# Kernel optimization log

Hardware: AMD Instinct MI355X
Metric: run time of the kernel (lower is better)

Reference implementation:

```python
import jax, jax.numpy as jnp
import numpy as np

V, D, H, L, S_MAX, FF = 32000, 1024, 16, 6, 1024, 4096
HD = D // H
EPS = 1e-5

def _ln(x, g, b):
    mu = jnp.mean(x, axis=-1, keepdims=True)
    var = jnp.mean((x - mu) ** 2, axis=-1, keepdims=True)
    return (x - mu) * jax.lax.rsqrt(var + EPS) * g + b

def setup_inputs() -> dict:
    key = jax.random.key(0)
    ks = jax.random.split(key, 12)
    std = 0.02
    d = {}
    d['x'] = jax.random.randint(ks[0], (2, 1024), 0, V)
    d['tok_emb'] = std * jax.random.normal(ks[1], (V, D), jnp.float32)
    d['pos_emb'] = std * jax.random.normal(ks[2], (S_MAX, D), jnp.float32)
    d['ln1_g'] = jnp.ones((L, D)); d['ln1_b'] = jnp.zeros((L, D))
    d['qkv_w'] = std * jax.random.normal(ks[3], (L, 3 * D, D), jnp.float32)
    d['qkv_b'] = jnp.zeros((L, 3 * D))
    d['proj_w'] = std * jax.random.normal(ks[4], (L, D, D), jnp.float32)
    d['proj_b'] = jnp.zeros((L, D))
    d['ln2_g'] = jnp.ones((L, D)); d['ln2_b'] = jnp.zeros((L, D))
    d['fc1_w'] = std * jax.random.normal(ks[5], (L, FF, D), jnp.float32)
    d['fc1_b'] = jnp.zeros((L, FF))
    d['fc2_w'] = std * jax.random.normal(ks[6], (L, D, FF), jnp.float32)
    d['fc2_b'] = jnp.zeros((L, D))
    d['lnf_g'] = jnp.ones((D,)); d['lnf_b'] = jnp.zeros((D,))
    d['head_w'] = std * jax.random.normal(ks[7], (V, D), jnp.float32)
    return d

def _gpt(x, tok_emb, pos_emb, ln1_g, ln1_b, qkv_w, qkv_b, proj_w, proj_b,
         ln2_g, ln2_b, fc1_w, fc1_b, fc2_w, fc2_b, lnf_g, lnf_b, head_w):
    B, S = x.shape
    h = tok_emb[x] + pos_emb[:S][None]  # (B,S,D)
    scale = HD ** -0.5
    causal = jnp.tril(jnp.ones((S, S), bool))
    neg_inf = jnp.finfo(h.dtype).min

    def block(h, p):
        l1g, l1b, qw, qb, pw, pb, l2g, l2b, f1w, f1b, f2w, f2b = p
        xn = _ln(h, l1g, l1b)
        qkv = xn @ qw.T + qb  # (B,S,3D)
        qkv = qkv.reshape(B, S, 3, H, HD).transpose(2, 0, 3, 1, 4)  # (3,B,H,S,HD)
        q, k, v = qkv[0], qkv[1], qkv[2]
        scores = jnp.einsum('bhqd,bhkd->bhqk', q, k) * scale
        scores = jnp.where(causal, scores, neg_inf)
        attn = jax.nn.softmax(scores, axis=-1)
        o = jnp.einsum('bhqk,bhkd->bhqd', attn, v)
        o = o.transpose(0, 2, 1, 3).reshape(B, S, D)
        h = h + (o @ pw.T + pb)
        xn = _ln(h, l2g, l2b)
        ff = jax.nn.gelu(xn @ f1w.T + f1b, approximate=False) @ f2w.T + f2b
        return h + ff, None

    params = (ln1_g, ln1_b, qkv_w, qkv_b, proj_w, proj_b,
              ln2_g, ln2_b, fc1_w, fc1_b, fc2_w, fc2_b)
    h, _ = jax.lax.scan(block, h, params)
    h = _ln(h, lnf_g, lnf_b)
    return h @ head_w.T  # (B,S,V)

def reference(x, tok_emb, pos_emb, ln1_g, ln1_b, qkv_w, qkv_b, proj_w, proj_b,
              ln2_g, ln2_b, fc1_w, fc1_b, fc2_w, fc2_b, lnf_g, lnf_b, head_w):
    return _gpt(x, tok_emb, pos_emb, ln1_g, ln1_b, qkv_w, qkv_b, proj_w, proj_b,
                ln2_g, ln2_b, fc1_w, fc1_b, fc2_w, fc2_b, lnf_g, lnf_b, head_w)
```

## Files before the change

kernel.cpp:

```cpp
#include <hip/hip_runtime.h>

typedef unsigned short u16;
typedef unsigned int   u32;
typedef __bf16 bf16x8 __attribute__((ext_vector_type(8)));
typedef float  f32x4  __attribute__((ext_vector_type(4)));

#define DEV __device__ __forceinline__

DEV u16 f2bf(float f) {
    u32 u = __builtin_bit_cast(u32, f);
    u32 r = u + 0x7FFFu + ((u >> 16) & 1u);
    return (u16)(r >> 16);
}

DEV void gload16(const void* g, void* l) {
    __builtin_amdgcn_global_load_lds((const __attribute__((address_space(1))) void*)g,
                                     (__attribute__((address_space(3))) void*)l, 16, 0, 0);
}

DEV int xcd_swz(int bid, int nwg) {
    int q = nwg >> 3, r = nwg & 7;
    int xcd = bid & 7, idx = bid >> 3;
    return (xcd < r ? xcd * (q + 1) : r * (q + 1) + (xcd - r) * q) + idx;
}

DEV int swz(int p) {
    int m = (((p >> 7) & 1) << 6) | (((p >> 9) & 1) << 5) | (((p >> 8) & 1) << 4);
    return p ^ m;
}

__global__ void cvt_k(const float* __restrict__ src, u16* __restrict__ dst, int n4) {
    int i = blockIdx.x * blockDim.x + threadIdx.x;
    int stride = gridDim.x * blockDim.x;
    for (; i < n4; i += stride) {
        float4 v = ((const float4*)src)[i];
        ushort4 u;
        u.x = f2bf(v.x); u.y = f2bf(v.y); u.z = f2bf(v.z); u.w = f2bf(v.w);
        ((ushort4*)dst)[i] = u;
    }
}

__global__ void cvt4_k(const float* __restrict__ s0, const float* __restrict__ s1,
                       const float* __restrict__ s2, const float* __restrict__ s3,
                       u16* __restrict__ dst, int n0, int n1, int n2, int n3) {
    int i = blockIdx.x * blockDim.x + threadIdx.x;
    int stride = gridDim.x * blockDim.x;
    int t0 = n0, t1 = t0 + n1, t2 = t1 + n2, t3 = t2 + n3;
    for (; i < t3; i += stride) {
        const float* s; int j;
        if (i < t0)      { s = s0; j = i; }
        else if (i < t1) { s = s1; j = i - t0; }
        else if (i < t2) { s = s2; j = i - t1; }
        else             { s = s3; j = i - t2; }
        float4 v = ((const float4*)s)[j];
        ushort4 u;
        u.x = f2bf(v.x); u.y = f2bf(v.y); u.z = f2bf(v.z); u.w = f2bf(v.w);
        ((ushort4*)dst)[i] = u;
    }
}

__global__ void embed_k(const int* __restrict__ x, const float* __restrict__ te,
                        const float* __restrict__ pe, float* __restrict__ h) {
    int row = blockIdx.x;
    int t = threadIdx.x;
    int tok = x[row];
    int s = row & 1023;
    float4 a = ((const float4*)(te + (size_t)tok * 1024))[t];
    float4 p = ((const float4*)(pe + (size_t)s * 1024))[t];
    a.x += p.x; a.y += p.y; a.z += p.z; a.w += p.w;
    ((float4*)(h + (size_t)row * 1024))[t] = a;
}

__global__ void ln_k(const float* __restrict__ in, const float* __restrict__ g,
                     const float* __restrict__ b, u16* __restrict__ out) {
    int row = blockIdx.x;
    int t = threadIdx.x;
    float4 v = ((const float4*)(in + (size_t)row * 1024))[t];
    float s = v.x + v.y + v.z + v.w;
    float s2 = v.x * v.x + v.y * v.y + v.z * v.z + v.w * v.w;
    #pragma unroll
    for (int msk = 1; msk < 64; msk <<= 1) {
        s  += __shfl_xor(s, msk);
        s2 += __shfl_xor(s2, msk);
    }
    __shared__ float ps[4], ps2[4];
    if ((t & 63) == 0) { ps[t >> 6] = s; ps2[t >> 6] = s2; }
    __syncthreads();
    s = ps[0] + ps[1] + ps[2] + ps[3];
    s2 = ps2[0] + ps2[1] + ps2[2] + ps2[3];
    float mu = s * (1.0f / 1024.0f);
    float var = s2 * (1.0f / 1024.0f) - mu * mu;
    float rstd = rsqrtf(var + 1e-5f);
    float4 gg = ((const float4*)g)[t];
    float4 bb = ((const float4*)b)[t];
    ushort4 o;
    o.x = f2bf((v.x - mu) * rstd * gg.x + bb.x);
    o.y = f2bf((v.y - mu) * rstd * gg.y + bb.y);
    o.z = f2bf((v.z - mu) * rstd * gg.z + bb.z);
    o.w = f2bf((v.w - mu) * rstd * gg.w + bb.w);
    ((ushort4*)out)[(size_t)row * 256 + t] = o;
}

__global__ void fuse2_k(const float* __restrict__ p0, const float* __restrict__ p1,
                        const float* __restrict__ bias, float* __restrict__ h) {
    int row = blockIdx.x;
    int t = threadIdx.x;
    size_t idx = (size_t)row * 256 + t;
    float4 a = ((const float4*)p0)[idx];
    float4 b = ((const float4*)p1)[idx];
    float4 c = ((const float4*)bias)[t];
    float4 v = ((const float4*)h)[idx];
    v.x += a.x + b.x + c.x;
    v.y += a.y + b.y + c.y;
    v.z += a.z + b.z + c.z;
    v.w += a.w + b.w + c.w;
    ((float4*)h)[idx] = v;
}

template<int PH>
DEV void phase_mma(const bf16x8 (&af)[2][2], const bf16x8 (&bfr)[4][2], f32x4 (&acc)[8][4]) {
    __builtin_amdgcn_s_barrier();
    asm volatile("s_waitcnt lgkmcnt(0)" ::: "memory");
    __builtin_amdgcn_sched_barrier(0);
    __builtin_amdgcn_s_setprio(1);
    #pragma unroll
    for (int ms = 0; ms < 2; ++ms)
        #pragma unroll
        for (int nj = 0; nj < 4; ++nj)
            #pragma unroll
            for (int kk = 0; kk < 2; ++kk)
                acc[PH * 2 + ms][nj] = __builtin_amdgcn_mfma_f32_16x16x32_bf16(
                    af[ms][kk], bfr[nj][kk], acc[PH * 2 + ms][nj], 0, 0, 0);
    __builtin_amdgcn_s_setprio(0);
}

template<int PH>
DEV void read_afrags(const char* Ab, int arow, int fr, int fq, bf16x8 (&af)[2][2]) {
    #pragma unroll
    for (int ms = 0; ms < 2; ++ms)
        #pragma unroll
        for (int kk = 0; kk < 2; ++kk) {
            int lin = (arow + (PH * 2 + ms) * 16 + fr) * 128 + kk * 64 + fq * 16;
            af[ms][kk] = *(const bf16x8*)(Ab + swz(lin));
        }
}

template<int BIAS, int OUTBF>
__global__ __launch_bounds__(512, 2)
void gemm8p(const u16* __restrict__ A, const u16* __restrict__ Bw,
            const float* __restrict__ bias,
            float* __restrict__ outf, u16* __restrict__ outb,
            int M, int N, int K) {
    __shared__ char lds[131072];
    char* ldsA = lds;
    char* ldsB = lds + 65536;
    const int t = threadIdx.x;
    const int w = t >> 6, l = t & 63;
    const int fr = l & 15, fq = l >> 4;
    const int wm = w >> 2, wn = w & 3;

    int bid = blockIdx.y * gridDim.x + blockIdx.x;
    int swzb = xcd_swz(bid, gridDim.x * gridDim.y);
    const int m0 = (swzb % gridDim.x) * 256;
    const int n0 = (swzb / gridDim.x) * 256;
    const int nt = K >> 6;
    const int arow = wm * 128;

    const u16* Asrc = A + (size_t)m0 * K;
    const u16* Bsrc = Bw + (size_t)n0 * K;

    size_t o00, o01, o10, o11;
    {
        int p;
        p = 0 * 16384 + 0 * 8192 + t * 16; o00 = (size_t)(p >> 7) * K + ((swz(p) & 127) >> 1);
        p = 0 * 16384 + 1 * 8192 + t * 16; o01 = (size_t)(p >> 7) * K + ((swz(p) & 127) >> 1);
        p = 1 * 16384 + 0 * 8192 + t * 16; o10 = (size_t)(p >> 7) * K + ((swz(p) & 127) >> 1);
        p = 1 * 16384 + 1 * 8192 + t * 16; o11 = (size_t)(p >> 7) * K + ((swz(p) & 127) >> 1);
    }
    const int wb = w * 1024;

    gload16(Asrc + o00, ldsA + wb);
    gload16(Asrc + o01, ldsA + 8192 + wb);
    gload16(Asrc + o10, ldsA + 16384 + wb);
    gload16(Asrc + o11, ldsA + 16384 + 8192 + wb);
    gload16(Bsrc + o00, ldsB + wb);
    gload16(Bsrc + o01, ldsB + 8192 + wb);
    gload16(Bsrc + o10, ldsB + 16384 + wb);
    gload16(Bsrc + o11, ldsB + 16384 + 8192 + wb);
    gload16(Bsrc + o00 + 64, ldsB + 32768 + wb);
    gload16(Bsrc + o01 + 64, ldsB + 32768 + 8192 + wb);
    gload16(Bsrc + o10 + 64, ldsB + 32768 + 16384 + wb);
    gload16(Bsrc + o11 + 64, ldsB + 32768 + 16384 + 8192 + wb);
    asm volatile("s_waitcnt vmcnt(4)" ::: "memory");
    __builtin_amdgcn_s_barrier();
    __builtin_amdgcn_sched_barrier(0);

    f32x4 acc[8][4] = {};

    for (int T = 0; T < nt; ++T) {
        const char* Ab = ldsA + (T & 1) * 32768;
        const char* Bb = ldsB + (T & 1) * 32768;
        char* Anx = ldsA + ((T + 1) & 1) * 32768;
        char* Bnx = ldsB + (T & 1) * 32768;
        const bool stA = (T + 1 < nt), stB = (T + 2 < nt);
        const size_t kA = (size_t)(T + 1) * 64, kB = (size_t)(T + 2) * 64;

        bf16x8 bfr[4][2], af[2][2];

        #pragma unroll
        for (int nj = 0; nj < 4; ++nj)
            #pragma unroll
            for (int kk = 0; kk < 2; ++kk) {
                int lin = (wn * 64 + nj * 16 + fr) * 128 + kk * 64 + fq * 16;
                bfr[nj][kk] = *(const bf16x8*)(Bb + swz(lin));
            }
        read_afrags<0>(Ab, arow, fr, fq, af);
        if (stA) {
            gload16(Asrc + o00 + kA, Anx + wb);
            gload16(Asrc + o01 + kA, Anx + 8192 + wb);
        }
        phase_mma<0>(af, bfr, acc);
        __builtin_amdgcn_s_barrier();

        read_afrags<1>(Ab, arow, fr, fq, af);
        if (stA) {
            gload16(Asrc + o10 + kA, Anx + 16384 + wb);
            gload16(Asrc + o11 + kA, Anx + 16384 + 8192 + wb);
        }
        phase_mma<1>(af, bfr, acc);
        __builtin_amdgcn_s_barrier();

        read_afrags<2>(Ab, arow, fr, fq, af);
        if (stB) {
            gload16(Bsrc + o00 + kB, Bnx + wb);
            gload16(Bsrc + o01 + kB, Bnx + 8192 + wb);
        }
        phase_mma<2>(af, bfr, acc);
        __builtin_amdgcn_s_barrier();

        read_afrags<3>(Ab, arow, fr, fq, af);
        if (stB) {
            gload16(Bsrc + o10 + kB, Bnx + 16384 + wb);
            gload16(Bsrc + o11 + kB, Bnx + 16384 + 8192 + wb);
        }
        phase_mma<3>(af, bfr, acc);
        if (stB)      asm volatile("s_waitcnt vmcnt(4)" ::: "memory");
        else if (stA) asm volatile("s_waitcnt vmcnt(0)" ::: "memory");
        __builtin_amdgcn_s_barrier();
        __builtin_amdgcn_sched_barrier(0);
    }

    #pragma unroll
    for (int mi = 0; mi < 8; ++mi) {
        #pragma unroll
        for (int nj = 0; nj < 4; ++nj) {
            #pragma unroll
            for (int r = 0; r < 4; ++r) {
                int row = m0 + wm * 128 + mi * 16 + fq * 4 + r;
                int col = n0 + wn * 64 + nj * 16 + fr;
                float v = acc[mi][nj][r];
                if (BIAS) v += bias[col];
                if (OUTBF) outb[(size_t)row * N + col] = f2bf(v);
                else       outf[(size_t)row * N + col] = v;
            }
        }
    }
}

template<int BIAS, int GELU_, int OUTBF, int SPLITK>
__global__ __launch_bounds__(512, 2)
void gemm4p(const u16* __restrict__ A, const u16* __restrict__ Bw,
            const float* __restrict__ bias,
            float* __restrict__ outf, u16* __restrict__ outb,
            int M, int N, int K) {
    __shared__ char lds[65536];
    char* ldsA = lds;
    char* ldsB = lds + 32768;
    const int t = threadIdx.x;
    const int w = t >> 6, l = t & 63;
    const int fr = l & 15, fq = l >> 4;
    const int wm = w >> 2, wn = w & 3;

    int bid = blockIdx.y * gridDim.x + blockIdx.x;
    int swzb = xcd_swz(bid, gridDim.x * gridDim.y);
    const int m0 = (swzb % gridDim.x) * 128;
    const int n0 = (swzb / gridDim.x) * 128;

    int kbase = 0, Keff = K;
    if (SPLITK) { Keff = K >> 1; kbase = blockIdx.z * Keff; }
    const int nt = Keff >> 6;

    const u16* Asrc = A + (size_t)m0 * K + kbase;
    const u16* Bsrc = Bw + (size_t)n0 * K + kbase;

    size_t o0, o1;
    {
        int p = t * 16;        o0 = (size_t)(p >> 7) * K + ((swz(p) & 127) >> 1);
        p = 8192 + t * 16;     o1 = (size_t)(p >> 7) * K + ((swz(p) & 127) >> 1);
    }
    const int wb = w * 1024;

    gload16(Asrc + o0, ldsA + wb);
    gload16(Asrc + o1, ldsA + 8192 + wb);
    gload16(Bsrc + o0, ldsB + wb);
    gload16(Bsrc + o1, ldsB + 8192 + wb);
    gload16(Bsrc + o0 + 64, ldsB + 16384 + wb);
    gload16(Bsrc + o1 + 64, ldsB + 16384 + 8192 + wb);
    asm volatile("s_waitcnt vmcnt(2)" ::: "memory");
    __builtin_amdgcn_s_barrier();
    __builtin_amdgcn_sched_barrier(0);

    f32x4 acc[4][2] = {};

    for (int T = 0; T < nt; ++T) {
        const char* Ab = ldsA + (T & 1) * 16384;
        const char* Bb = ldsB + (T & 1) * 16384;
        char* Anx = ldsA + ((T + 1) & 1) * 16384;
        char* Bnx = ldsB + (T & 1) * 16384;
        const bool stA = (T + 1 < nt), stB = (T + 2 < nt);
        const size_t kA = (size_t)(T + 1) * 64, kB = (size_t)(T + 2) * 64;

        bf16x8 bfr[2][2], af[2][2];

        #pragma unroll
        for (int nj = 0; nj < 2; ++nj)
            #pragma unroll
            for (int kk = 0; kk < 2; ++kk) {
                int lin = (wn * 32 + nj * 16 + fr) * 128 + kk * 64 + fq * 16;
                bfr[nj][kk] = *(const bf16x8*)(Bb + swz(lin));
            }
        #pragma unroll
        for (int ms = 0; ms < 2; ++ms)
            #pragma unroll
            for (int kk = 0; kk < 2; ++kk) {
                int lin = (wm * 64 + ms * 16 + fr) * 128 + kk * 64 + fq * 16;
                af[ms][kk] = *(const bf16x8*)(Ab + swz(lin));
            }
        if (stA) {
            gload16(Asrc + o0 + kA, Anx + wb);
            gload16(Asrc + o1 + kA, Anx + 8192 + wb);
        }
        __builtin_amdgcn_s_barrier();
        asm volatile("s_waitcnt lgkmcnt(0)" ::: "memory");
        __builtin_amdgcn_sched_barrier(0);
        __builtin_amdgcn_s_setprio(1);
        #pragma unroll
        for (int ms = 0; ms < 2; ++ms)
            #pragma unroll
            for (int nj = 0; nj < 2; ++nj)
                #pragma unroll
                for (int kk = 0; kk < 2; ++kk)
                    acc[ms][nj] = __builtin_amdgcn_mfma_f32_16x16x32_bf16(
                        af[ms][kk], bfr[nj][kk], acc[ms][nj], 0, 0, 0);
        __builtin_amdgcn_s_setprio(0);
        __builtin_amdgcn_s_barrier();

        #pragma unroll
        for (int ms = 0; ms < 2; ++ms)
            #pragma unroll
            for (int kk = 0; kk < 2; ++kk) {
                int lin = (wm * 64 + (2 + ms) * 16 + fr) * 128 + kk * 64 + fq * 16;
                af[ms][kk] = *(const bf16x8*)(Ab + swz(lin));
            }
        if (stB) {
            gload16(Bsrc + o0 + kB, Bnx + wb);
            gload16(Bsrc + o1 + kB, Bnx + 8192 + wb);
        }
        __builtin_amdgcn_s_barrier();
        asm volatile("s_waitcnt lgkmcnt(0)" ::: "memory");
        __builtin_amdgcn_sched_barrier(0);
        __builtin_amdgcn_s_setprio(1);
        #pragma unroll
        for (int ms = 0; ms < 2; ++ms)
            #pragma unroll
            for (int nj = 0; nj < 2; ++nj)
                #pragma unroll
                for (int kk = 0; kk < 2; ++kk)
                    acc[2 + ms][nj] = __builtin_amdgcn_mfma_f32_16x16x32_bf16(
                        af[ms][kk], bfr[nj][kk], acc[2 + ms][nj], 0, 0, 0);
        __builtin_amdgcn_s_setprio(0);
        if (stB)      asm volatile("s_waitcnt vmcnt(2)" ::: "memory");
        else if (stA) asm volatile("s_waitcnt vmcnt(0)" ::: "memory");
        __builtin_amdgcn_s_barrier();
        __builtin_amdgcn_sched_barrier(0);
    }

    float* op = outf;
    if (SPLITK) op = outf + (size_t)blockIdx.z * M * N;

    #pragma unroll
    for (int mi = 0; mi < 4; ++mi) {
        #pragma unroll
        for (int nj = 0; nj < 2; ++nj) {
            #pragma unroll
            for (int r = 0; r < 4; ++r) {
                int row = m0 + wm * 64 + mi * 16 + fq * 4 + r;
                int col = n0 + wn * 32 + nj * 16 + fr;
                float v = acc[mi][nj][r];
                if (BIAS) v += bias[col];
                if (GELU_) v = 0.5f * v * (1.0f + erff(v * 0.70710678118f));
                if (OUTBF) outb[(size_t)row * N + col] = f2bf(v);
                else       op[(size_t)row * N + col] = v;
            }
        }
    }
}

template<int BM, int BN, int BIAS, int GELU_, int RES, int OUTBF, int SPLITK>
__global__ void gemm_db(const u16* __restrict__ A, const u16* __restrict__ Bw,
                        const float* __restrict__ bias, const float* __restrict__ res,
                        float* __restrict__ outf, u16* __restrict__ outb,
                        int M, int N, int K) {
    constexpr int MR = BM / 32;
    constexpr int NR = BN / 32;
    constexpr int AL = BM / 64;
    constexpr int BL = BN / 64;
    __shared__ u16 lA[2][BM * 32];
    __shared__ u16 lB[2][BN * 32];
    const int t = threadIdx.x;
    const int w = t >> 6, l = t & 63;

    int bid = blockIdx.y * gridDim.x + blockIdx.x;
    int swzb = xcd_swz(bid, gridDim.x * gridDim.y);
    const int m0 = (swzb % gridDim.x) * BM;
    const int n0 = (swzb / gridDim.x) * BN;

    int kbase = 0, Keff = K;
    if (SPLITK) { Keff = K >> 1; kbase = blockIdx.z * Keff; }
    const int nt = Keff >> 5;

    const int wr = (w >> 1) * (BM / 2), wc = (w & 1) * (BN / 2);
    const int fr = l & 15, fq = l >> 4;
    const int g0 = w * 64 + l;

    const int srow = g0 >> 2, scol = (g0 & 3) * 8;

    f32x4 acc[MR][NR] = {};

    #pragma unroll
    for (int i = 0; i < AL; ++i)
        gload16(A + (size_t)(m0 + srow + i * 64) * K + kbase + scol, lA[0] + (srow + i * 64) * 32 + scol);
    #pragma unroll
    for (int i = 0; i < BL; ++i)
        gload16(Bw + (size_t)(n0 + srow + i * 64) * K + kbase + scol, lB[0] + (srow + i * 64) * 32 + scol);
    __syncthreads();

    for (int T = 0; T < nt; ++T) {
        const int cur = T & 1, nxt = cur ^ 1;
        if (T + 1 < nt) {
            const int kk = kbase + (T + 1) * 32;
            #pragma unroll
            for (int i = 0; i < AL; ++i)
                gload16(A + (size_t)(m0 + srow + i * 64) * K + kk + scol, lA[nxt] + (srow + i * 64) * 32 + scol);
            #pragma unroll
            for (int i = 0; i < BL; ++i)
                gload16(Bw + (size_t)(n0 + srow + i * 64) * K + kk + scol, lB[nxt] + (srow + i * 64) * 32 + scol);
        }
        bf16x8 af[MR], bfv[NR];
        #pragma unroll
        for (int mi = 0; mi < MR; ++mi)
            af[mi] = *(const bf16x8*)(lA[cur] + (wr + mi * 16 + fr) * 32 + fq * 8);
        #pragma unroll
        for (int ni = 0; ni < NR; ++ni)
            bfv[ni] = *(const bf16x8*)(lB[cur] + (wc + ni * 16 + fr) * 32 + fq * 8);
        #pragma unroll
        for (int mi = 0; mi < MR; ++mi)
            #pragma unroll
            for (int ni = 0; ni < NR; ++ni)
                acc[mi][ni] = __builtin_amdgcn_mfma_f32_16x16x32_bf16(af[mi], bfv[ni], acc[mi][ni], 0, 0, 0);
        __syncthreads();
    }

    float* op = outf;
    if (SPLITK) op = outf + (size_t)blockIdx.z * M * N;

    #pragma unroll
    for (int mi = 0; mi < MR; ++mi) {
        #pragma unroll
        for (int ni = 0; ni < NR; ++ni) {
            #pragma unroll
            for (int r = 0; r < 4; ++r) {
                int row = m0 + wr + mi * 16 + fq * 4 + r;
                int col = n0 + wc + ni * 16 + fr;
                float v = acc[mi][ni][r];
                if (BIAS) v += bias[col];
                if (GELU_) v = 0.5f * v * (1.0f + erff(v * 0.70710678118f));
                if (RES) v += res[(size_t)row * N + col];
                if (OUTBF) outb[(size_t)row * N + col] = f2bf(v);
                else       op[(size_t)row * N + col] = v;
            }
        }
    }
}

__global__ __launch_bounds__(512, 2)
void attn_k(const u16* __restrict__ qkv, u16* __restrict__ o) {
    __shared__ u16 lK[64 * 64];
    __shared__ u16 lV[64 * 64];
    __shared__ u16 lP[8 * 16 * 64];
    const int t = threadIdx.x;
    const int w = t >> 6, l = t & 63;
    const int fr = l & 15, fq = l >> 4;

    int swzb = xcd_swz(blockIdx.x, gridDim.x);
    const int qb = 7 - (swzb & 7);
    const int hh = (swzb >> 3) & 15;
    const int b  = swzb >> 7;
    const int q0 = qb * 128;
    const int qw = q0 + w * 16;

    const u16* srcK;
    {
        int p = t * 16;
        int L = swz(p);
        srcK = qkv + ((size_t)(b * 1024) + (L >> 7)) * 3072 + 1024 + hh * 64 + ((L & 127) >> 1);
    }

    bf16x8 qf[2];
    {
        size_t base = ((size_t)(b * 1024) + qw + fr) * 3072 + hh * 64;
        qf[0] = *(const bf16x8*)(qkv + base + fq * 8);
        qf[1] = *(const bf16x8*)(qkv + base + 32 + fq * 8);
    }

    float m_run[4], l_run[4];
    f32x4 acc_o[4] = {};
    #pragma unroll
    for (int r = 0; r < 4; ++r) { m_run[r] = -__builtin_inff(); l_run[r] = 0.0f; }

    for (int kv0 = 0; kv0 < q0 + 128; kv0 += 64) {
        gload16(srcK + (size_t)kv0 * 3072, (char*)lK + w * 1024);
        {
            int kv = t >> 3, d0 = (t & 7) * 8;
            const u32* gv = (const u32*)(qkv + ((size_t)(b * 1024) + kv0 + kv) * 3072 + 2048 + hh * 64 + d0);
            u32 v0 = gv[0], v1 = gv[1], v2 = gv[2], v3 = gv[3];
            u16 e[8] = { (u16)v0, (u16)(v0 >> 16), (u16)v1, (u16)(v1 >> 16),
                         (u16)v2, (u16)(v2 >> 16), (u16)v3, (u16)(v3 >> 16) };
            #pragma unroll
            for (int j = 0; j < 8; ++j) {
                int pv = ((d0 + j) * 64 + kv) * 2;
                *(u16*)((char*)lV + swz(pv)) = e[j];
            }
        }
        __syncthreads();

        const bool active = (kv0 <= qw + 15);
        if (active) {
            f32x4 accs[4] = {};
            #pragma unroll
            for (int nt = 0; nt < 4; ++nt) {
                #pragma unroll
                for (int ks = 0; ks < 2; ++ks) {
                    int pk = ((nt * 16 + fr) * 64 + ks * 32 + fq * 8) * 2;
                    bf16x8 kf = *(const bf16x8*)((const char*)lK + swz(pk));
                    accs[nt] = __builtin_amdgcn_mfma_f32_16x16x32_bf16(qf[ks], kf, accs[nt], 0, 0, 0);
                }
            }

            float p[4][4], mx[4], rs[4];
            #pragma unroll
            for (int r = 0; r < 4; ++r) {
                int qg = qw + fq * 4 + r;
                float m = -__builtin_inff();
                #pragma unroll
                for (int nt = 0; nt < 4; ++nt) {
                    int kvg = kv0 + nt * 16 + fr;
                    float s = (kvg <= qg) ? accs[nt][r] * 0.125f : -__builtin_inff();
                    p[nt][r] = s;
                    m = fmaxf(m, s);
                }
                mx[r] = m;
            }
            #pragma unroll
            for (int msk = 1; msk < 16; msk <<= 1) {
                #pragma unroll
                for (int r = 0; r < 4; ++r) mx[r] = fmaxf(mx[r], __shfl_xor(mx[r], msk));
            }
            float mnew[4], alpha[4];
            #pragma unroll
            for (int r = 0; r < 4; ++r) {
                mnew[r] = fmaxf(m_run[r], mx[r]);
                alpha[r] = __expf(m_run[r] - mnew[r]);
                float s = 0.0f;
                #pragma unroll
                for (int nt = 0; nt < 4; ++nt) {
                    float pv = __expf(p[nt][r] - mnew[r]);
                    p[nt][r] = pv;
                    s += pv;
                }
                rs[r] = s;
            }
            #pragma unroll
            for (int msk = 1; msk < 16; msk <<= 1) {
                #pragma unroll
                for (int r = 0; r < 4; ++r) rs[r] += __shfl_xor(rs[r], msk);
            }
            #pragma unroll
            for (int r = 0; r < 4; ++r) {
                l_run[r] = l_run[r] * alpha[r] + rs[r];
                m_run[r] = mnew[r];
            }
            #pragma unroll
            for (int nt = 0; nt < 4; ++nt)
                #pragma unroll
                for (int r = 0; r < 4; ++r) acc_o[nt][r] *= alpha[r];

            #pragma unroll
            for (int nt = 0; nt < 4; ++nt)
                #pragma unroll
                for (int r = 0; r < 4; ++r) {
                    int pp = (w * 1024 + (fq * 4 + r) * 64 + nt * 16 + fr) * 2;
                    *(u16*)((char*)lP + swz(pp)) = f2bf(p[nt][r]);
                }

            bf16x8 pa[2];
            #pragma unroll
            for (int ks = 0; ks < 2; ++ks) {
                int ppr = (w * 1024 + fr * 64 + ks * 32 + fq * 8) * 2;
                pa[ks] = *(const bf16x8*)((const char*)lP + swz(ppr));
            }
            #pragma unroll
            for (int nt = 0; nt < 4; ++nt) {
                #pragma unroll
                for (int ks = 0; ks < 2; ++ks) {
                    int pvr = ((nt * 16 + fr) * 64 + ks * 32 + fq * 8) * 2;
                    bf16x8 vf = *(const bf16x8*)((const char*)lV + swz(pvr));
                    acc_o[nt] = __builtin_amdgcn_mfma_f32_16x16x32_bf16(pa[ks], vf, acc_o[nt], 0, 0, 0);
                }
            }
        }
        __syncthreads();
    }

    #pragma unroll
    for (int nt = 0; nt < 4; ++nt) {
        #pragma unroll
        for (int r = 0; r < 4; ++r) {
            int qg = qw + fq * 4 + r;
            int d = nt * 16 + fr;
            float ov = acc_o[nt][r] / l_run[r];
            o[((size_t)(b * 1024) + qg) * 1024 + hh * 64 + d] = f2bf(ov);
        }
    }
}

extern "C" void kernel_launch(void* const* d_in, const int* in_sizes, int n_in,
                              void* d_out, int out_size, void* d_ws, size_t ws_size,
                              hipStream_t stream) {
    const int*   x       = (const int*)  d_in[0];
    const float* tok_emb = (const float*)d_in[1];
    const float* pos_emb = (const float*)d_in[2];
    const float* ln1_g   = (const float*)d_in[3];
    const float* ln1_b   = (const float*)d_in[4];
    const float* qkv_w   = (const float*)d_in[5];
    const float* qkv_b   = (const float*)d_in[6];
    const float* proj_w  = (const float*)d_in[7];
    const float* proj_b  = (const float*)d_in[8];
    const float* ln2_g   = (const float*)d_in[9];
    const float* ln2_b   = (const float*)d_in[10];
    const float* fc1_w   = (const float*)d_in[11];
    const float* fc1_b   = (const float*)d_in[12];
    const float* fc2_w   = (const float*)d_in[13];
    const float* fc2_b   = (const float*)d_in[14];
    const float* lnf_g   = (const float*)d_in[15];
    const float* lnf_b   = (const float*)d_in[16];
    const float* head_w  = (const float*)d_in[17];
    float* out = (float*)d_out;

    char* ws = (char*)d_ws;
    float* h   = (float*)(ws + 0);
    u16*   xn  = (u16*)(ws + 8388608);
    u16*   qkv = (u16*)(ws + 12582912);
    u16*   ob  = (u16*)(ws + 25165824);
    u16*   ff  = (u16*)(ws + 29360128);
    u16*   wq  = (u16*)(ws + 46137344);
    float* pbuf = (float*)(ws + 12582912);

    u16* wqkv = wq;
    u16* wproj = wqkv + 3072 * 1024;
    u16* wfc1  = wproj + 1024 * 1024;
    u16* wfc2  = wfc1 + 4096 * 1024;

    const int M = 2048;

    embed_k<<<dim3(2048), 256, 0, stream>>>(x, tok_emb, pos_emb, h);

    for (int lyr = 0; lyr < 6; ++lyr) {
        cvt4_k<<<dim3(2048), 256, 0, stream>>>(
            qkv_w + (size_t)lyr * 3072 * 1024, proj_w + (size_t)lyr * 1024 * 1024,
            fc1_w + (size_t)lyr * 4096 * 1024, fc2_w + (size_t)lyr * 1024 * 4096,
            wq, 3072 * 256, 1024 * 256, 4096 * 256, 4096 * 256);
        ln_k<<<dim3(2048), 256, 0, stream>>>(h, ln1_g + lyr * 1024, ln1_b + lyr * 1024, xn);
        gemm4p<1, 0, 1, 0><<<dim3(16, 24), 512, 0, stream>>>(
            xn, wqkv, qkv_b + lyr * 3072, nullptr, qkv, M, 3072, 1024);
        attn_k<<<dim3(256), 512, 0, stream>>>(qkv, ob);
        gemm_db<64, 64, 1, 0, 1, 0, 0><<<dim3(32, 16), 256, 0, stream>>>(
            ob, wproj, proj_b + lyr * 1024, h, h, nullptr, M, 1024, 1024);
        ln_k<<<dim3(2048), 256, 0, stream>>>(h, ln2_g + lyr * 1024, ln2_b + lyr * 1024, xn);
        gemm4p<1, 1, 1, 0><<<dim3(16, 32), 512, 0, stream>>>(
            xn, wfc1, fc1_b + lyr * 4096, nullptr, ff, M, 4096, 1024);
        gemm4p<0, 0, 0, 1><<<dim3(16, 8, 2), 512, 0, stream>>>(
            ff, wfc2, nullptr, pbuf, nullptr, M, 1024, 4096);
        fuse2_k<<<dim3(2048), 256, 0, stream>>>(
            pbuf, pbuf + (size_t)M * 1024, fc2_b + lyr * 1024, h);
    }

    ln_k<<<dim3(2048), 256, 0, stream>>>(h, lnf_g, lnf_b, xn);
    cvt_k<<<dim3(2048), 256, 0, stream>>>(head_w, wq, 32000 * 1024 / 4);
    gemm8p<0, 0><<<dim3(8, 125), 512, 0, stream>>>(
        xn, wq, nullptr, out, nullptr, M, 32000, 1024);
}
```

Measured before the change: 1.256 ms.

## Fuse LayerNorm into embedding and residual-reduce kernels; use gemm4p for head

LayerNorm is computed inside the embedding kernel and inside the split-K residual reduction kernel, which now also produces the next layer's normalized input (or the final LN). This removes the standalone LN launches and the extra passes over the fp32 hidden state. The vocabulary projection switches from the large-tile gemm8p kernel to the smaller-tile gemm4p kernel, and gemm8p is deleted. Smaller tiles raise global traffic for the head GEMM but may improve occupancy and load balance.

```diff
diff --git a/kernel.cpp b/kernel.cpp
--- a/kernel.cpp
+++ b/kernel.cpp
@@ -59,23 +59,8 @@
     }
 }
 
-__global__ void embed_k(const int* __restrict__ x, const float* __restrict__ te,
-                        const float* __restrict__ pe, float* __restrict__ h) {
-    int row = blockIdx.x;
-    int t = threadIdx.x;
-    int tok = x[row];
-    int s = row & 1023;
-    float4 a = ((const float4*)(te + (size_t)tok * 1024))[t];
-    float4 p = ((const float4*)(pe + (size_t)s * 1024))[t];
-    a.x += p.x; a.y += p.y; a.z += p.z; a.w += p.w;
-    ((float4*)(h + (size_t)row * 1024))[t] = a;
-}
-
-__global__ void ln_k(const float* __restrict__ in, const float* __restrict__ g,
-                     const float* __restrict__ b, u16* __restrict__ out) {
-    int row = blockIdx.x;
-    int t = threadIdx.x;
-    float4 v = ((const float4*)(in + (size_t)row * 1024))[t];
+DEV void ln_store(float4 v, const float* __restrict__ g, const float* __restrict__ b,
+                  u16* __restrict__ out, int row, int t) {
     float s = v.x + v.y + v.z + v.w;
     float s2 = v.x * v.x + v.y * v.y + v.z * v.z + v.w * v.w;
     #pragma unroll
@@ -101,170 +86,46 @@
     ((ushort4*)out)[(size_t)row * 256 + t] = o;
 }
 
-__global__ void fuse2_k(const float* __restrict__ p0, const float* __restrict__ p1,
-                        const float* __restrict__ bias, float* __restrict__ h) {
+__global__ void ln_k(const float* __restrict__ in, const float* __restrict__ g,
+                     const float* __restrict__ b, u16* __restrict__ out) {
+    int row = blockIdx.x;
+    int t = threadIdx.x;
+    float4 v = ((const float4*)(in + (size_t)row * 1024))[t];
+    ln_store(v, g, b, out, row, t);
+}
+
+__global__ void embed_ln_k(const int* __restrict__ x, const float* __restrict__ te,
+                           const float* __restrict__ pe, float* __restrict__ h,
+                           const float* __restrict__ g, const float* __restrict__ b,
+                           u16* __restrict__ xn) {
+    int row = blockIdx.x;
+    int t = threadIdx.x;
+    int tok = x[row];
+    int s = row & 1023;
+    float4 a = ((const float4*)(te + (size_t)tok * 1024))[t];
+    float4 p = ((const float4*)(pe + (size_t)s * 1024))[t];
+    a.x += p.x; a.y += p.y; a.z += p.z; a.w += p.w;
+    ((float4*)(h + (size_t)row * 1024))[t] = a;
+    ln_store(a, g, b, xn, row, t);
+}
+
+__global__ void fuse2ln_k(const float* __restrict__ p0, const float* __restrict__ p1,
+                          const float* __restrict__ bias, float* __restrict__ h,
+                          const float* __restrict__ g, const float* __restrict__ b,
+                          u16* __restrict__ xn) {
     int row = blockIdx.x;
     int t = threadIdx.x;
     size_t idx = (size_t)row * 256 + t;
     float4 a = ((const float4*)p0)[idx];
-    float4 b = ((const float4*)p1)[idx];
+    float4 bb = ((const float4*)p1)[idx];
     float4 c = ((const float4*)bias)[t];
     float4 v = ((const float4*)h)[idx];
-    v.x += a.x + b.x + c.x;
-    v.y += a.y + b.y + c.y;
-    v.z += a.z + b.z + c.z;
-    v.w += a.w + b.w + c.w;
+    v.x += a.x + bb.x + c.x;
+    v.y += a.y + bb.y + c.y;
+    v.z += a.z + bb.z + c.z;
+    v.w += a.w + bb.w + c.w;
     ((float4*)h)[idx] = v;
-}
-
-template<int PH>
-DEV void phase_mma(const bf16x8 (&af)[2][2], const bf16x8 (&bfr)[4][2], f32x4 (&acc)[8][4]) {
-    __builtin_amdgcn_s_barrier();
-    asm volatile("s_waitcnt lgkmcnt(0)" ::: "memory");
-    __builtin_amdgcn_sched_barrier(0);
-    __builtin_amdgcn_s_setprio(1);
-    #pragma unroll
-    for (int ms = 0; ms < 2; ++ms)
-        #pragma unroll
-        for (int nj = 0; nj < 4; ++nj)
-            #pragma unroll
-            for (int kk = 0; kk < 2; ++kk)
-                acc[PH * 2 + ms][nj] = __builtin_amdgcn_mfma_f32_16x16x32_bf16(
-                    af[ms][kk], bfr[nj][kk], acc[PH * 2 + ms][nj], 0, 0, 0);
-    __builtin_amdgcn_s_setprio(0);
-}
-
-template<int PH>
-DEV void read_afrags(const char* Ab, int arow, int fr, int fq, bf16x8 (&af)[2][2]) {
-    #pragma unroll
-    for (int ms = 0; ms < 2; ++ms)
-        #pragma unroll
-        for (int kk = 0; kk < 2; ++kk) {
-            int lin = (arow + (PH * 2 + ms) * 16 + fr) * 128 + kk * 64 + fq * 16;
-            af[ms][kk] = *(const bf16x8*)(Ab + swz(lin));
-        }
-}
-
-template<int BIAS, int OUTBF>
-__global__ __launch_bounds__(512, 2)
-void gemm8p(const u16* __restrict__ A, const u16* __restrict__ Bw,
-            const float* __restrict__ bias,
-            float* __restrict__ outf, u16* __restrict__ outb,
-            int M, int N, int K) {
-    __shared__ char lds[131072];
-    char* ldsA = lds;
-    char* ldsB = lds + 65536;
-    const int t = threadIdx.x;
-    const int w = t >> 6, l = t & 63;
-    const int fr = l & 15, fq = l >> 4;
-    const int wm = w >> 2, wn = w & 3;
-
-    int bid = blockIdx.y * gridDim.x + blockIdx.x;
-    int swzb = xcd_swz(bid, gridDim.x * gridDim.y);
-    const int m0 = (swzb % gridDim.x) * 256;
-    const int n0 = (swzb / gridDim.x) * 256;
-    const int nt = K >> 6;
-    const int arow = wm * 128;
-
-    const u16* Asrc = A + (size_t)m0 * K;
-    const u16* Bsrc = Bw + (size_t)n0 * K;
-
-    size_t o00, o01, o10, o11;
-    {
-        int p;
-        p = 0 * 16384 + 0 * 8192 + t * 16; o00 = (size_t)(p >> 7) * K + ((swz(p) & 127) >> 1);
-        p = 0 * 16384 + 1 * 8192 + t * 16; o01 = (size_t)(p >> 7) * K + ((swz(p) & 127) >> 1);
-        p = 1 * 16384 + 0 * 8192 + t * 16; o10 = (size_t)(p >> 7) * K + ((swz(p) & 127) >> 1);
-        p = 1 * 16384 + 1 * 8192 + t * 16; o11 = (size_t)(p >> 7) * K + ((swz(p) & 127) >> 1);
-    }
-    const int wb = w * 1024;
-
-    gload16(Asrc + o00, ldsA + wb);
-    gload16(Asrc + o01, ldsA + 8192 + wb);
-    gload16(Asrc + o10, ldsA + 16384 + wb);
-    gload16(Asrc + o11, ldsA + 16384 + 8192 + wb);
-    gload16(Bsrc + o00, ldsB + wb);
-    gload16(Bsrc + o01, ldsB + 8192 + wb);
-    gload16(Bsrc + o10, ldsB + 16384 + wb);
-    gload16(Bsrc + o11, ldsB + 16384 + 8192 + wb);
-    gload16(Bsrc + o00 + 64, ldsB + 32768 + wb);
-    gload16(Bsrc + o01 + 64, ldsB + 32768 + 8192 + wb);
-    gload16(Bsrc + o10 + 64, ldsB + 32768 + 16384 + wb);
-    gload16(Bsrc + o11 + 64, ldsB + 32768 + 16384 + 8192 + wb);
-    asm volatile("s_waitcnt vmcnt(4)" ::: "memory");
-    __builtin_amdgcn_s_barrier();
-    __builtin_amdgcn_sched_barrier(0);
-
-    f32x4 acc[8][4] = {};
-
-    for (int T = 0; T < nt; ++T) {
-        const char* Ab = ldsA + (T & 1) * 32768;
-        const char* Bb = ldsB + (T & 1) * 32768;
-        char* Anx = ldsA + ((T + 1) & 1) * 32768;
-        char* Bnx = ldsB + (T & 1) * 32768;
-        const bool stA = (T + 1 < nt), stB = (T + 2 < nt);
-        const size_t kA = (size_t)(T + 1) * 64, kB = (size_t)(T + 2) * 64;
-
-        bf16x8 bfr[4][2], af[2][2];
-
-        #pragma unroll
-        for (int nj = 0; nj < 4; ++nj)
-            #pragma unroll
-            for (int kk = 0; kk < 2; ++kk) {
-                int lin = (wn * 64 + nj * 16 + fr) * 128 + kk * 64 + fq * 16;
-                bfr[nj][kk] = *(const bf16x8*)(Bb + swz(lin));
-            }
-        read_afrags<0>(Ab, arow, fr, fq, af);
-        if (stA) {
-            gload16(Asrc + o00 + kA, Anx + wb);
-            gload16(Asrc + o01 + kA, Anx + 8192 + wb);
-        }
-        phase_mma<0>(af, bfr, acc);
-        __builtin_amdgcn_s_barrier();
-
-        read_afrags<1>(Ab, arow, fr, fq, af);
-        if (stA) {
-            gload16(Asrc + o10 + kA, Anx + 16384 + wb);
-            gload16(Asrc + o11 + kA, Anx + 16384 + 8192 + wb);
-        }
-        phase_mma<1>(af, bfr, acc);
-        __builtin_amdgcn_s_barrier();
-
-        read_afrags<2>(Ab, arow, fr, fq, af);
-        if (stB) {
-            gload16(Bsrc + o00 + kB, Bnx + wb);
-            gload16(Bsrc + o01 + kB, Bnx + 8192 + wb);
-        }
-        phase_mma<2>(af, bfr, acc);
-        __builtin_amdgcn_s_barrier();
-
-        read_afrags<3>(Ab, arow, fr, fq, af);
-        if (stB) {
-            gload16(Bsrc + o10 + kB, Bnx + 16384 + wb);
-            gload16(Bsrc + o11 + kB, Bnx + 16384 + 8192 + wb);
-        }
-        phase_mma<3>(af, bfr, acc);
-        if (stB)      asm volatile("s_waitcnt vmcnt(4)" ::: "memory");
-        else if (stA) asm volatile("s_waitcnt vmcnt(0)" ::: "memory");
-        __builtin_amdgcn_s_barrier();
-        __builtin_amdgcn_sched_barrier(0);
-    }
-
-    #pragma unroll
-    for (int mi = 0; mi < 8; ++mi) {
-        #pragma unroll
-        for (int nj = 0; nj < 4; ++nj) {
-            #pragma unroll
-            for (int r = 0; r < 4; ++r) {
-                int row = m0 + wm * 128 + mi * 16 + fq * 4 + r;
-                int col = n0 + wn * 64 + nj * 16 + fr;
-                float v = acc[mi][nj][r];
-                if (BIAS) v += bias[col];
-                if (OUTBF) outb[(size_t)row * N + col] = f2bf(v);
-                else       outf[(size_t)row * N + col] = v;
-            }
-        }
-    }
+    ln_store(v, g, b, xn, row, t);
 }
 
 template<int BIAS, int GELU_, int OUTBF, int SPLITK>
@@ -683,14 +544,13 @@
 
     const int M = 2048;
 
-    embed_k<<<dim3(2048), 256, 0, stream>>>(x, tok_emb, pos_emb, h);
+    embed_ln_k<<<dim3(2048), 256, 0, stream>>>(x, tok_emb, pos_emb, h, ln1_g, ln1_b, xn);
 
     for (int lyr = 0; lyr < 6; ++lyr) {
         cvt4_k<<<dim3(2048), 256, 0, stream>>>(
             qkv_w + (size_t)lyr * 3072 * 1024, proj_w + (size_t)lyr * 1024 * 1024,
             fc1_w + (size_t)lyr * 4096 * 1024, fc2_w + (size_t)lyr * 1024 * 4096,
             wq, 3072 * 256, 1024 * 256, 4096 * 256, 4096 * 256);
-        ln_k<<<dim3(2048), 256, 0, stream>>>(h, ln1_g + lyr * 1024, ln1_b + lyr * 1024, xn);
         gemm4p<1, 0, 1, 0><<<dim3(16, 24), 512, 0, stream>>>(
             xn, wqkv, qkv_b + lyr * 3072, nullptr, qkv, M, 3072, 1024);
         attn_k<<<dim3(256), 512, 0, stream>>>(qkv, ob);
@@ -701,12 +561,13 @@
             xn, wfc1, fc1_b + lyr * 4096, nullptr, ff, M, 4096, 1024);
         gemm4p<0, 0, 0, 1><<<dim3(16, 8, 2), 512, 0, stream>>>(
             ff, wfc2, nullptr, pbuf, nullptr, M, 1024, 4096);
-        fuse2_k<<<dim3(2048), 256, 0, stream>>>(
-            pbuf, pbuf + (size_t)M * 1024, fc2_b + lyr * 1024, h);
-    }
-
-    ln_k<<<dim3(2048), 256, 0, stream>>>(h, lnf_g, lnf_b, xn);
+        const float* g = (lyr < 5) ? (ln1_g + (lyr + 1) * 1024) : lnf_g;
+        const float* b = (lyr < 5) ? (ln1_b + (lyr + 1) * 1024) : lnf_b;
+        fuse2ln_k<<<dim3(2048), 256, 0, stream>>>(
+            pbuf, pbuf + (size_t)M * 1024, fc2_b + lyr * 1024, h, g, b, xn);
+    }
+
     cvt_k<<<dim3(2048), 256, 0, stream>>>(head_w, wq, 32000 * 1024 / 4);
-    gemm8p<0, 0><<<dim3(8, 125), 512, 0, stream>>>(
+    gemm4p<0, 0, 0, 0><<<dim3(16, 250), 512, 0, stream>>>(
         xn, wq, nullptr, out, nullptr, M, 32000, 1024);
 }
```

New measurement: 1.248 ms. Within noise of the previous version (-0.7%).
